# Performance work log

Hardware: AMD Instinct MI355X
Metric: run time of the kernel (lower is better)

Reference implementation:

```python
import jax, jax.numpy as jnp
import numpy as np

D_MODEL = 1024
H = 16
D_K = D_MODEL // H
B, S = 2, 2048


def setup_inputs() -> dict:
    key = jax.random.key(0)
    ks = jax.random.split(key, 13)
    sc = 1.0 / np.sqrt(D_MODEL)
    inp = {
        "x": jax.random.normal(ks[0], (B, S, D_MODEL), jnp.float32),
        "q": jax.random.normal(ks[1], (B, S, D_MODEL), jnp.float32),
        "k": jax.random.normal(ks[2], (B, S, D_MODEL), jnp.float32),
        "v": jax.random.normal(ks[3], (B, S, D_MODEL), jnp.float32),
        "mask": jnp.ones((1, 1, S, S), jnp.int32),
        "w_q": jax.random.normal(ks[4], (D_MODEL, D_MODEL), jnp.float32) * sc,
        "b_q": jax.random.normal(ks[5], (D_MODEL,), jnp.float32) * sc,
        "w_k": jax.random.normal(ks[6], (D_MODEL, D_MODEL), jnp.float32) * sc,
        "b_k": jax.random.normal(ks[7], (D_MODEL,), jnp.float32) * sc,
        "w_v": jax.random.normal(ks[8], (D_MODEL, D_MODEL), jnp.float32) * sc,
        "b_v": jax.random.normal(ks[9], (D_MODEL,), jnp.float32) * sc,
        "w_o": jax.random.normal(ks[10], (D_MODEL, D_MODEL), jnp.float32) * sc,
        "b_o": jax.random.normal(ks[11], (D_MODEL,), jnp.float32) * sc,
    }
    return inp


def reference(x, q, k, v, mask, w_q, b_q, w_k, b_k, w_v, b_v, w_o, b_o):
    # Faithful to source bugs: value projected with w_k (not w_v);
    # mask and dropout have no effect (non-in-place / broken calls); x unused.
    query = q @ w_q.T + b_q                     # [B,S,D]
    key_p = k @ w_k.T + b_k                     # [B,S,D]
    value = v @ w_k.T + b_k                     # BUG in source: uses w_k
    # split heads -> [B,H,S,d_k]
    qh = query.reshape(B, S, H, D_K).transpose(0, 2, 1, 3)
    kh = key_p.reshape(B, S, H, D_K).transpose(0, 2, 1, 3)
    vh = value.reshape(B, S, H, D_K).transpose(0, 2, 1, 3)
    scores = jnp.einsum("bhqd,bhkd->bhqk", qh, kh) / jnp.sqrt(jnp.float32(D_K))
    attn = jax.nn.softmax(scores, axis=-1)      # [B,H,S,S]
    out = jnp.einsum("bhqk,bhkd->bhqd", attn, vh)
    out = out.transpose(0, 2, 1, 3).reshape(B, S, D_MODEL)
    return out @ w_o.T + b_o
```

## Files before the change

kernel.cpp:

```cpp
#include <hip/hip_runtime.h>

typedef unsigned short u16;
typedef __attribute__((ext_vector_type(8))) __bf16 bf16x8;
typedef __attribute__((ext_vector_type(4))) float f32x4;
typedef __attribute__((ext_vector_type(16))) float f32x16;
typedef __attribute__((ext_vector_type(8))) u16 u16x8;
typedef __attribute__((ext_vector_type(4))) u16 u16x4;
typedef __attribute__((ext_vector_type(4))) unsigned u32x4;

#define AS1 __attribute__((address_space(1)))
#define AS3 __attribute__((address_space(3)))

#if __has_builtin(__builtin_amdgcn_exp2f)
#define EXP2(x) __builtin_amdgcn_exp2f(x)
#else
#define EXP2(x) exp2f(x)
#endif

__device__ __forceinline__ u16 f2bf(float f) {
  union { float f; unsigned u; } cv; cv.f = f;
  return (u16)((cv.u + 0x7FFFu + ((cv.u >> 16) & 1u)) >> 16);
}

__device__ __forceinline__ void gload16(const void* g, void* l) {
  __builtin_amdgcn_global_load_lds((AS1 const void*)g, (AS3 void*)l, 16, 0, 0);
}

__device__ __forceinline__ unsigned cvtpk(float lo, float hi_) {
  unsigned d;
  asm("v_cvt_pk_bf16_f32 %0, %1, %2" : "=v"(d) : "v"(lo), "v"(hi_));
  return d;
}

__device__ __forceinline__ int lds_off(int row, int chunk) {
  return row * 64 + ((chunk ^ (row & 7)) << 3);
}

__global__ void cvt_kernel(const float* __restrict__ s0, u16* __restrict__ d0, int n0,
                           const float* __restrict__ s1, u16* __restrict__ d1, int n1,
                           const float* __restrict__ s2, u16* __restrict__ d2, int n2,
                           const float* __restrict__ s3, u16* __restrict__ d3, int n3,
                           const float* __restrict__ s4, u16* __restrict__ d4, int n4,
                           const float* __restrict__ s5, u16* __restrict__ d5, int n5) {
  const float* s; u16* d; int n;
  switch (blockIdx.y) {
    case 0: s = s0; d = d0; n = n0; break;
    case 1: s = s1; d = d1; n = n1; break;
    case 2: s = s2; d = d2; n = n2; break;
    case 3: s = s3; d = d3; n = n3; break;
    case 4: s = s4; d = d4; n = n4; break;
    default: s = s5; d = d5; n = n5; break;
  }
  const int stride = gridDim.x * blockDim.x;
  for (int i = blockIdx.x * blockDim.x + threadIdx.x; i < n; i += stride) {
    const float4* p = (const float4*)(s + (size_t)i * 8);
    float4 a = p[0], b = p[1];
    u16x8 r;
    r[0] = f2bf(a.x); r[1] = f2bf(a.y); r[2] = f2bf(a.z); r[3] = f2bf(a.w);
    r[4] = f2bf(b.x); r[5] = f2bf(b.y); r[6] = f2bf(b.z); r[7] = f2bf(b.w);
    *(u16x8*)(d + (size_t)i * 8) = r;
  }
}

__device__ __forceinline__ void gemm_core(const u16* __restrict__ A,
                                          const u16* __restrict__ Bm,
                                          u16* As, u16* Bs,
                                          int rowBase, int colBase,
                                          f32x4 acc[4][4]) {
  const int tid = threadIdx.x;
  const int lane = tid & 63, w = tid >> 6;
  const int wr = w >> 1, wc = w & 1;
  const int l15 = lane & 15, g = lane >> 4;

  for (int kt = 0; kt < 1024; kt += 32) {
    __syncthreads();
#pragma unroll
    for (int it = 0; it < 2; ++it) {
      int e = it * 256 + tid;
      int r = e >> 2, kc = (e & 3) << 3;
      gload16(A + (((size_t)(rowBase + r)) << 10) + kt + kc, As + e * 8);
      gload16(Bm + (((size_t)(colBase + r)) << 10) + kt + kc, Bs + e * 8);
    }
    __syncthreads();
    bf16x8 a[4], b[4];
#pragma unroll
    for (int mt = 0; mt < 4; ++mt)
      a[mt] = *(const bf16x8*)(As + (wr * 64 + mt * 16 + l15) * 32 + g * 8);
#pragma unroll
    for (int nt = 0; nt < 4; ++nt)
      b[nt] = *(const bf16x8*)(Bs + (wc * 64 + nt * 16 + l15) * 32 + g * 8);
#pragma unroll
    for (int mt = 0; mt < 4; ++mt)
#pragma unroll
      for (int nt = 0; nt < 4; ++nt)
        acc[mt][nt] = __builtin_amdgcn_mfma_f32_16x16x32_bf16(a[mt], b[nt], acc[mt][nt], 0, 0, 0);
  }
}

__global__ __launch_bounds__(256)
void proj_gemm(const u16* __restrict__ qb, const u16* __restrict__ kb, const u16* __restrict__ vb,
               const u16* __restrict__ wqb, const u16* __restrict__ wkb,
               const float* __restrict__ b_q, const float* __restrict__ b_k,
               u16* __restrict__ Qp, u16* __restrict__ Kp, u16* __restrict__ VTp) {
  __shared__ __align__(16) u16 As[128 * 32];
  __shared__ __align__(16) u16 Bs[128 * 32];

  const u16* A; const u16* Bm; const float* bias; u16* C; int mode;
  float scale = 1.0f;
  if (blockIdx.z == 0)      { A = qb; Bm = wqb; bias = b_q; C = Qp;  mode = 0; scale = 0.18033688011112042f; }
  else if (blockIdx.z == 1) { A = kb; Bm = wkb; bias = b_k; C = Kp;  mode = 0; }
  else                      { A = vb; Bm = wkb; bias = b_k; C = VTp; mode = 1; }

  const int rowBase = blockIdx.x * 128;
  const int colBase = blockIdx.y * 128;
  f32x4 acc[4][4];
  const f32x4 z4 = {0.f, 0.f, 0.f, 0.f};
#pragma unroll
  for (int i = 0; i < 4; ++i)
#pragma unroll
    for (int j = 0; j < 4; ++j) acc[i][j] = z4;

  gemm_core(A, Bm, As, Bs, rowBase, colBase, acc);

  const int tid = threadIdx.x;
  const int lane = tid & 63, w = tid >> 6;
  const int wr = w >> 1, wc = w & 1;
  const int l15 = lane & 15, g = lane >> 4;
#pragma unroll
  for (int mt = 0; mt < 4; ++mt)
#pragma unroll
    for (int nt = 0; nt < 4; ++nt) {
      int col = colBase + wc * 64 + nt * 16 + l15;
      float bia = bias[col];
#pragma unroll
      for (int r = 0; r < 4; ++r) {
        int row = rowBase + wr * 64 + mt * 16 + g * 4 + r;
        float val = (acc[mt][nt][r] + bia) * scale;
        if (mode == 0) {
          C[(((size_t)row) << 10) + col] = f2bf(val);
        } else {
          int bb = row >> 11, s = row & 2047;
          int s2 = s ^ ((((s >> 2) ^ (s >> 3)) & 1) * 12);
          int hh = col >> 6, d = col & 63;
          C[((((size_t)(bb * 16 + hh)) << 6) + d) * 2048 + s2] = f2bf(val);
        }
      }
    }
}

__global__ __launch_bounds__(256)
void out_gemm(const u16* __restrict__ AO, const u16* __restrict__ wob,
              const float* __restrict__ b_o, float* __restrict__ C) {
  __shared__ __align__(16) u16 As[64 * 32];
  __shared__ __align__(16) u16 Bs[128 * 32];
  const int rowBase = blockIdx.x * 64;
  const int colBase = blockIdx.y * 128;

  const int tid = threadIdx.x;
  const int lane = tid & 63, w = tid >> 6;
  const int wr = w >> 1, wc = w & 1;
  const int l15 = lane & 15, g = lane >> 4;

  f32x4 acc[2][4];
  const f32x4 z4 = {0.f, 0.f, 0.f, 0.f};
#pragma unroll
  for (int i = 0; i < 2; ++i)
#pragma unroll
    for (int j = 0; j < 4; ++j) acc[i][j] = z4;

  for (int kt = 0; kt < 1024; kt += 32) {
    __syncthreads();
    {
      int r = tid >> 2, kc = (tid & 3) << 3;
      gload16(AO + (((size_t)(rowBase + r)) << 10) + kt + kc, As + tid * 8);
    }
#pragma unroll
    for (int it = 0; it < 2; ++it) {
      int e = it * 256 + tid;
      int r = e >> 2, kc = (e & 3) << 3;
      gload16(wob + (((size_t)(colBase + r)) << 10) + kt + kc, Bs + e * 8);
    }
    __syncthreads();
    bf16x8 a[2], b[4];
#pragma unroll
    for (int mt = 0; mt < 2; ++mt)
      a[mt] = *(const bf16x8*)(As + (wr * 32 + mt * 16 + l15) * 32 + g * 8);
#pragma unroll
    for (int nt = 0; nt < 4; ++nt)
      b[nt] = *(const bf16x8*)(Bs + (wc * 64 + nt * 16 + l15) * 32 + g * 8);
#pragma unroll
    for (int mt = 0; mt < 2; ++mt)
#pragma unroll
      for (int nt = 0; nt < 4; ++nt)
        acc[mt][nt] = __builtin_amdgcn_mfma_f32_16x16x32_bf16(a[mt], b[nt], acc[mt][nt], 0, 0, 0);
  }

#pragma unroll
  for (int mt = 0; mt < 2; ++mt)
#pragma unroll
    for (int nt = 0; nt < 4; ++nt) {
      int col = colBase + wc * 64 + nt * 16 + l15;
      float bia = b_o[col];
#pragma unroll
      for (int r = 0; r < 4; ++r) {
        int row = rowBase + wr * 32 + mt * 16 + g * 4 + r;
        C[(((size_t)row) << 10) + col] = acc[mt][nt][r] + bia;
      }
    }
}

template <int KS4>
__device__ __forceinline__ void pv_step(const f32x16& sv, int hi, const u16* Vt, int l31,
                                        f32x16& o0, f32x16& o1) {
  constexpr int B = (KS4 & 1) * 8;
  u32x4 pd;
  pd[0] = cvtpk(sv[B + 0], sv[B + 1]);
  pd[1] = cvtpk(sv[B + 2], sv[B + 3]);
  pd[2] = cvtpk(sv[B + 4], sv[B + 5]);
  pd[3] = cvtpk(sv[B + 6], sv[B + 7]);
  bf16x8 pfrag = __builtin_bit_cast(bf16x8, pd);
  bf16x8 av0 = *(const bf16x8*)(Vt + lds_off(l31, 2 * KS4 + hi));
  bf16x8 av1 = *(const bf16x8*)(Vt + lds_off(32 + l31, 2 * KS4 + hi));
  o0 = __builtin_amdgcn_mfma_f32_32x32x16_bf16(av0, pfrag, o0, 0, 0, 0);
  o1 = __builtin_amdgcn_mfma_f32_32x32x16_bf16(av1, pfrag, o1, 0, 0, 0);
}

__global__ __launch_bounds__(512, 4)
void flash_attn(const u16* __restrict__ Qp, const u16* __restrict__ Kp,
                const u16* __restrict__ VT, u16* __restrict__ AO) {
  __shared__ __align__(16) u16 KB[2][2][64 * 64];
  __shared__ __align__(16) u16 VB[2][2][64 * 64];
  __shared__ float shML[2][256];

  const int tid = threadIdx.x;
  const int lane = tid & 63;
  const int w = tid >> 6;
  const int h = w >> 2;
  const int wq = w & 3;
  const int l31 = lane & 31;
  const int hi = lane >> 5;
  const int tid256 = tid & 255;

  const int flat = blockIdx.x + (blockIdx.y << 4);
  const int wgid = (flat & 7) * 64 + (flat >> 3);
  const int bh = wgid >> 4;
  const int qblk = wgid & 15;
  const int b = bh >> 4, hd = bh & 15;
  const int q = qblk * 128 + wq * 32 + l31;

  const size_t qrow = ((size_t)(b * 2048 + q)) << 10;
  const u16* Kbase = Kp + (((size_t)(b * 2048)) << 10) + hd * 64;
  const u16* Vbase = VT + (((size_t)(bh * 64)) << 11);

  const int sr = tid256 >> 3;
  const int sc = (tid256 & 7) ^ (sr & 7);

  auto stage = [&](int tt, int buf) {
    const int kv0 = tt * 64;
    gload16(Kbase + (((size_t)(kv0 + sr)) << 10) + sc * 8, &KB[h][buf][tid256 * 8]);
    gload16(Kbase + (((size_t)(kv0 + 32 + sr)) << 10) + sc * 8, &KB[h][buf][2048 + tid256 * 8]);
    gload16(Vbase + sr * 2048 + kv0 + sc * 8, &VB[h][buf][tid256 * 8]);
    gload16(Vbase + (32 + sr) * 2048 + kv0 + sc * 8, &VB[h][buf][2048 + tid256 * 8]);
  };

  stage(h * 16, 0);

  bf16x8 qf[4];
#pragma unroll
  for (int ks = 0; ks < 4; ++ks)
    qf[ks] = *(const bf16x8*)(Qp + qrow + hd * 64 + ks * 16 + hi * 8);

  float m = -1e30f, l = 0.f;
  f32x16 o0, o1;
#pragma unroll
  for (int i = 0; i < 16; ++i) { o0[i] = 0.f; o1[i] = 0.f; }

  for (int lt = 0; lt < 16; ++lt) {
    const int cb = lt & 1;
    asm volatile("s_waitcnt vmcnt(0)" ::: "memory");
    __builtin_amdgcn_sched_barrier(0);
    __builtin_amdgcn_s_barrier();
    __builtin_amdgcn_sched_barrier(0);
    if (lt < 15) stage(h * 16 + lt + 1, cb ^ 1);

    const u16* Kt = &KB[h][cb][0];
    const u16* Vt = &VB[h][cb][0];

    f32x16 s0, s1;
#pragma unroll
    for (int i = 0; i < 16; ++i) { s0[i] = 0.f; s1[i] = 0.f; }
#pragma unroll
    for (int ks = 0; ks < 4; ++ks) {
      bf16x8 ak0 = *(const bf16x8*)(Kt + lds_off(l31, 2 * ks + hi));
      bf16x8 ak1 = *(const bf16x8*)(Kt + lds_off(32 + l31, 2 * ks + hi));
      s0 = __builtin_amdgcn_mfma_f32_32x32x16_bf16(ak0, qf[ks], s0, 0, 0, 0);
      s1 = __builtin_amdgcn_mfma_f32_32x32x16_bf16(ak1, qf[ks], s1, 0, 0, 0);
    }

    f32x16 mm;
#pragma unroll
    for (int i = 0; i < 16; ++i) mm[i] = fmaxf(s0[i], s1[i]);
#pragma unroll
    for (int i = 0; i < 8; ++i) mm[i] = fmaxf(mm[i], mm[i + 8]);
#pragma unroll
    for (int i = 0; i < 4; ++i) mm[i] = fmaxf(mm[i], mm[i + 4]);
    float pm = fmaxf(fmaxf(mm[0], mm[1]), fmaxf(mm[2], mm[3]));
    pm = fmaxf(pm, __shfl_xor(pm, 32));

    if (!__all(pm - m <= 11.0f)) {
      float mn = fmaxf(m, pm);
      float fr = EXP2(m - mn);
      m = mn;
      l *= fr;
#pragma unroll
      for (int i = 0; i < 16; ++i) { o0[i] *= fr; o1[i] *= fr; }
    }

#pragma unroll
    for (int i = 0; i < 16; ++i) {
      s0[i] = EXP2(s0[i] - m);
      s1[i] = EXP2(s1[i] - m);
    }
#pragma unroll
    for (int i = 0; i < 16; ++i) mm[i] = s0[i] + s1[i];
#pragma unroll
    for (int i = 0; i < 8; ++i) mm[i] += mm[i + 8];
#pragma unroll
    for (int i = 0; i < 4; ++i) mm[i] += mm[i + 4];
    float ps = (mm[0] + mm[1]) + (mm[2] + mm[3]);
    ps += __shfl_xor(ps, 32);
    l += ps;

    pv_step<0>(s0, hi, Vt, l31, o0, o1);
    pv_step<1>(s0, hi, Vt, l31, o0, o1);
    pv_step<2>(s1, hi, Vt, l31, o0, o1);
    pv_step<3>(s1, hi, Vt, l31, o0, o1);
  }

  const int wl = wq * 64 + lane;
  float* shO0 = (float*)&KB[1][0][0];
  float* shO1 = (float*)&VB[1][0][0];
  if (h == 1) {
#pragma unroll
    for (int i = 0; i < 16; ++i) {
      shO0[i * 256 + wl] = o0[i];
      shO1[i * 256 + wl] = o1[i];
    }
    shML[0][wl] = m;
    shML[1][wl] = l;
  }
  __syncthreads();
  if (h == 0) {
    float mb = shML[0][wl], lb = shML[1][wl];
    float M = fmaxf(m, mb);
    float f0 = EXP2(m - M), f1 = EXP2(mb - M);
    float linv = 1.0f / (l * f0 + lb * f1);
#pragma unroll
    for (int i = 0; i < 16; ++i) {
      o0[i] = o0[i] * f0 + shO0[i * 256 + wl] * f1;
      o1[i] = o1[i] * f0 + shO1[i * 256 + wl] * f1;
    }
#pragma unroll
    for (int dt = 0; dt < 2; ++dt) {
      const f32x16& oo = dt ? o1 : o0;
#pragma unroll
      for (int g = 0; g < 4; ++g) {
        u16x4 pk;
#pragma unroll
        for (int r = 0; r < 4; ++r) pk[r] = f2bf(oo[g * 4 + r] * linv);
        const int d = dt * 32 + g * 8 + hi * 4;
        *(u16x4*)(AO + qrow + hd * 64 + d) = pk;
      }
    }
  }
}

extern "C" void kernel_launch(void* const* d_in, const int* in_sizes, int n_in,
                              void* d_out, int out_size, void* d_ws, size_t ws_size,
                              hipStream_t stream) {
  const float* q   = (const float*)d_in[1];
  const float* k   = (const float*)d_in[2];
  const float* v   = (const float*)d_in[3];
  const float* w_q = (const float*)d_in[5];
  const float* b_q = (const float*)d_in[6];
  const float* w_k = (const float*)d_in[7];
  const float* b_k = (const float*)d_in[8];
  const float* w_o = (const float*)d_in[11];
  const float* b_o = (const float*)d_in[12];
  float* out = (float*)d_out;

  u16* qb  = (u16*)d_ws;
  u16* kb  = qb  + 4194304;
  u16* vb  = kb  + 4194304;
  u16* wqb = vb  + 4194304;
  u16* wkb = wqb + 1048576;
  u16* wob = wkb + 1048576;
  u16* Qp  = wob + 1048576;
  u16* Kp  = Qp  + 4194304;
  u16* VTp = Kp  + 4194304;
  u16* AO  = qb;

  cvt_kernel<<<dim3(512, 6, 1), 256, 0, stream>>>(
      q, qb, 524288, k, kb, 524288, v, vb, 524288,
      w_q, wqb, 131072, w_k, wkb, 131072, w_o, wob, 131072);

  proj_gemm<<<dim3(32, 8, 3), 256, 0, stream>>>(qb, kb, vb, wqb, wkb, b_q, b_k, Qp, Kp, VTp);

  flash_attn<<<dim3(16, 32, 1), 512, 0, stream>>>(Qp, Kp, VTp, AO);

  out_gemm<<<dim3(64, 8, 1), 256, 0, stream>>>(AO, wob, b_o, out);
}
```

Before: 125.8 us.

## Double-buffer LDS tiles in projection and output GEMMs to overlap loads

Both GEMM kernels now keep two LDS buffers and issue the global-to-LDS loads for the next K tile before running MFMAs on the current one. This leaves one barrier per iteration instead of two and lets the memory latency hide behind the matrix math. The cost is double the LDS per block, which may lower occupancy. Correctness now depends on the vmcnt wait and barrier ordering, since a buffer is overwritten one iteration after it was read.

```diff
diff --git a/kernel.cpp b/kernel.cpp
--- a/kernel.cpp
+++ b/kernel.cpp
@@ -72,23 +72,35 @@
   const int wr = w >> 1, wc = w & 1;
   const int l15 = lane & 15, g = lane >> 4;
 
-  for (int kt = 0; kt < 1024; kt += 32) {
-    __syncthreads();
+  auto stage = [&](int kt, int buf) {
 #pragma unroll
     for (int it = 0; it < 2; ++it) {
       int e = it * 256 + tid;
       int r = e >> 2, kc = (e & 3) << 3;
-      gload16(A + (((size_t)(rowBase + r)) << 10) + kt + kc, As + e * 8);
-      gload16(Bm + (((size_t)(colBase + r)) << 10) + kt + kc, Bs + e * 8);
-    }
-    __syncthreads();
+      gload16(A + (((size_t)(rowBase + r)) << 10) + kt + kc, As + buf * 4096 + e * 8);
+      gload16(Bm + (((size_t)(colBase + r)) << 10) + kt + kc, Bs + buf * 4096 + e * 8);
+    }
+  };
+
+  stage(0, 0);
+
+  for (int i = 0; i < 32; ++i) {
+    const int cb = i & 1;
+    asm volatile("s_waitcnt vmcnt(0)" ::: "memory");
+    __builtin_amdgcn_sched_barrier(0);
+    __builtin_amdgcn_s_barrier();
+    __builtin_amdgcn_sched_barrier(0);
+    if (i < 31) stage((i + 1) * 32, cb ^ 1);
+
+    const u16* Ab = As + cb * 4096;
+    const u16* Bb = Bs + cb * 4096;
     bf16x8 a[4], b[4];
 #pragma unroll
     for (int mt = 0; mt < 4; ++mt)
-      a[mt] = *(const bf16x8*)(As + (wr * 64 + mt * 16 + l15) * 32 + g * 8);
+      a[mt] = *(const bf16x8*)(Ab + (wr * 64 + mt * 16 + l15) * 32 + g * 8);
 #pragma unroll
     for (int nt = 0; nt < 4; ++nt)
-      b[nt] = *(const bf16x8*)(Bs + (wc * 64 + nt * 16 + l15) * 32 + g * 8);
+      b[nt] = *(const bf16x8*)(Bb + (wc * 64 + nt * 16 + l15) * 32 + g * 8);
 #pragma unroll
     for (int mt = 0; mt < 4; ++mt)
 #pragma unroll
@@ -102,8 +114,8 @@
                const u16* __restrict__ wqb, const u16* __restrict__ wkb,
                const float* __restrict__ b_q, const float* __restrict__ b_k,
                u16* __restrict__ Qp, u16* __restrict__ Kp, u16* __restrict__ VTp) {
-  __shared__ __align__(16) u16 As[128 * 32];
-  __shared__ __align__(16) u16 Bs[128 * 32];
+  __shared__ __align__(16) u16 As[2][128 * 32];
+  __shared__ __align__(16) u16 Bs[2][128 * 32];
 
   const u16* A; const u16* Bm; const float* bias; u16* C; int mode;
   float scale = 1.0f;
@@ -120,7 +132,7 @@
 #pragma unroll
     for (int j = 0; j < 4; ++j) acc[i][j] = z4;
 
-  gemm_core(A, Bm, As, Bs, rowBase, colBase, acc);
+  gemm_core(A, Bm, &As[0][0], &Bs[0][0], rowBase, colBase, acc);
 
   const int tid = threadIdx.x;
   const int lane = tid & 63, w = tid >> 6;
@@ -151,8 +163,8 @@
 __global__ __launch_bounds__(256)
 void out_gemm(const u16* __restrict__ AO, const u16* __restrict__ wob,
               const float* __restrict__ b_o, float* __restrict__ C) {
-  __shared__ __align__(16) u16 As[64 * 32];
-  __shared__ __align__(16) u16 Bs[128 * 32];
+  __shared__ __align__(16) u16 As[2][64 * 32];
+  __shared__ __align__(16) u16 Bs[2][128 * 32];
   const int rowBase = blockIdx.x * 64;
   const int colBase = blockIdx.y * 128;
 
@@ -161,33 +173,43 @@
   const int wr = w >> 1, wc = w & 1;
   const int l15 = lane & 15, g = lane >> 4;
 
-  f32x4 acc[2][4];
-  const f32x4 z4 = {0.f, 0.f, 0.f, 0.f};
-#pragma unroll
-  for (int i = 0; i < 2; ++i)
-#pragma unroll
-    for (int j = 0; j < 4; ++j) acc[i][j] = z4;
-
-  for (int kt = 0; kt < 1024; kt += 32) {
-    __syncthreads();
+  auto stage = [&](int kt, int buf) {
     {
       int r = tid >> 2, kc = (tid & 3) << 3;
-      gload16(AO + (((size_t)(rowBase + r)) << 10) + kt + kc, As + tid * 8);
+      gload16(AO + (((size_t)(rowBase + r)) << 10) + kt + kc, &As[buf][tid * 8]);
     }
 #pragma unroll
     for (int it = 0; it < 2; ++it) {
       int e = it * 256 + tid;
       int r = e >> 2, kc = (e & 3) << 3;
-      gload16(wob + (((size_t)(colBase + r)) << 10) + kt + kc, Bs + e * 8);
-    }
-    __syncthreads();
+      gload16(wob + (((size_t)(colBase + r)) << 10) + kt + kc, &Bs[buf][e * 8]);
+    }
+  };
+
+  f32x4 acc[2][4];
+  const f32x4 z4 = {0.f, 0.f, 0.f, 0.f};
+#pragma unroll
+  for (int i = 0; i < 2; ++i)
+#pragma unroll
+    for (int j = 0; j < 4; ++j) acc[i][j] = z4;
+
+  stage(0, 0);
+
+  for (int i = 0; i < 32; ++i) {
+    const int cb = i & 1;
+    asm volatile("s_waitcnt vmcnt(0)" ::: "memory");
+    __builtin_amdgcn_sched_barrier(0);
+    __builtin_amdgcn_s_barrier();
+    __builtin_amdgcn_sched_barrier(0);
+    if (i < 31) stage((i + 1) * 32, cb ^ 1);
+
     bf16x8 a[2], b[4];
 #pragma unroll
     for (int mt = 0; mt < 2; ++mt)
-      a[mt] = *(const bf16x8*)(As + (wr * 32 + mt * 16 + l15) * 32 + g * 8);
+      a[mt] = *(const bf16x8*)(&As[cb][(wr * 32 + mt * 16 + l15) * 32 + g * 8]);
 #pragma unroll
     for (int nt = 0; nt < 4; ++nt)
-      b[nt] = *(const bf16x8*)(Bs + (wc * 64 + nt * 16 + l15) * 32 + g * 8);
+      b[nt] = *(const bf16x8*)(&Bs[cb][(wc * 64 + nt * 16 + l15) * 32 + g * 8]);
 #pragma unroll
     for (int mt = 0; mt < 2; ++mt)
 #pragma unroll
```

After: 130.9 us. 1.04x slower.
